# Kernel tuning notes

Measured on AMD Instinct MI355X. Metric: run time of the kernel, lower is better.

## Reference

```python
import jax, jax.numpy as jnp
import numpy as np
import math

ATTN_SCALE = 1.0 / math.sqrt(128.0)
NEG_INF = float(np.finfo(np.float32).min)


def get_slopes(n_heads: int) -> np.ndarray:
    # ALiBi head-specific slopes, geometric series; handles non-power-of-2 heads.
    n = 2 ** math.floor(math.log2(n_heads))
    m_0 = 2.0 ** (-8.0 / n)
    m = m_0 ** np.arange(1, 1 + n, dtype=np.float64)
    if n < n_heads:
        m_hat_0 = 2.0 ** (-4.0 / n)
        m_hat = m_hat_0 ** np.arange(1, 1 + 2 * (n_heads - n), 2, dtype=np.float64)
        m = np.concatenate([m, m_hat])
    return m.astype(np.float32).reshape(1, -1, 1, 1)  # [1, h, 1, 1]


def setup_inputs() -> dict:
    key = jax.random.key(0)
    kq, kk, kv = jax.random.split(key, 3)
    b, h, s, d = 4, 16, 2048, 128
    q = jax.random.normal(kq, (b, h, s, d), dtype=jnp.float32)
    k = jax.random.normal(kk, (b, h, s, d), dtype=jnp.float32)
    v = jax.random.normal(kv, (b, h, s, d), dtype=jnp.float32)
    return {"q": q, "k": k, "v": v}


def reference(q, k, v):
    b, h, s_q, d = q.shape
    s_kv = k.shape[2]
    # scores: [b, h, s_q, s_kv]
    s = jnp.einsum('bhqd,bhkd->bhqk', q, k) * ATTN_SCALE
    # ALiBi: (j - i) * slope_h, added after scaling
    rel = (jnp.arange(s_kv, dtype=q.dtype)[None, :]
           - jnp.arange(s_q, dtype=q.dtype)[:, None])  # [s_q, s_kv]
    slopes = jnp.asarray(get_slopes(h), dtype=q.dtype)  # [1, h, 1, 1]
    s = s + rel[None, None, :, :] * slopes
    # causal mask: positions j > i get -inf
    causal = jnp.arange(s_kv)[None, :] > jnp.arange(s_q)[:, None]  # [s_q, s_kv]
    s = jnp.where(causal[None, None, :, :], jnp.array(-jnp.inf, dtype=s.dtype), s)
    p = jax.nn.softmax(s, axis=-1)
    o = jnp.einsum('bhqk,bhkd->bhqd', p, v)
    return o
```

## Files before the change

### kernel.cpp

```cpp
#include <hip/hip_runtime.h>
#include <math.h>

#define S_LEN 2048
#define DHEAD 128
#define NHEAD 16
#define QBLK  256
#define KVBLK 64
#define ATT_SCALE 0.08838834764831845f
#define LOG2E 1.4426950408889634f
#define SHIFT2 11.5f

#define KP 136
#define VP 72

typedef __attribute__((ext_vector_type(4))) float f32x4;
typedef __attribute__((ext_vector_type(8))) short s16x8;
typedef __attribute__((ext_vector_type(2))) int   i32x2;

__device__ __forceinline__ int pk2(float lo, float hi) {
  int d;
  asm("v_cvt_pk_bf16_f32 %0, %1, %2" : "=v"(d) : "v"(lo), "v"(hi));
  return d;
}

#define BARRIER() do {                                   \
    asm volatile("s_waitcnt lgkmcnt(0)" ::: "memory");   \
    __builtin_amdgcn_s_barrier();                        \
  } while (0)


__global__ __launch_bounds__(512, 2)
void alibi_attn_fwd(const float* __restrict__ Qg, const float* __restrict__ Kg,
                    const float* __restrict__ Vg, float* __restrict__ Og)
{
  __shared__ __align__(16) short kt[2][KVBLK * KP];
  __shared__ __align__(16) short vt[3][DHEAD * VP];

  const int tid  = threadIdx.x;
  const int lane = tid & 63;
  const int w    = tid >> 6;
  const int l16  = lane & 15;
  const int lg   = lane >> 4;

  const int n    = blockIdx.x;
  const int bh   = n & 63;
  const int p    = n >> 6;
  const int head = bh & (NHEAD - 1);

  const size_t base = (size_t)bh * S_LEN * DHEAD;
  const float* Q = Qg + base;
  const float* K = Kg + base;
  const float* V = Vg + base;
  float*       O = Og + base;

  const float slope2 = exp2f(-0.5f * (float)(head + 1)) * LOG2E;
  float cn16[4], rsv[4];
  #pragma unroll
  for (int x = 0; x < 4; ++x) { cn16[x] = (float)(16 * x) * slope2; rsv[x] = (float)x * slope2; }

  s16x8 ones;
  #pragma unroll
  for (int jj = 0; jj < 8; ++jj) ones[jj] = (short)0x3f80;

  const f32x4 zero4 = {0.f, 0.f, 0.f, 0.f};

  const int qt0 = 7 - p, qt1 = p;
  const int qb0 = qt0 * QBLK, qb1 = qt1 * QBLK;
  const int n0  = 4 * (qt0 + 1);
  const int NT  = n0 + 4 * (qt1 + 1);

  const int kr  = tid >> 3;
  const int d0k = 16 * (tid & 7);
  const int grp = tid & 15, vnt = grp >> 2, vg = grp & 3;
  const int Rv  = 16 * vnt + 4 * vg;
  const int dv  = 4 * (tid >> 4);
  const int vslotb = 32 * (vnt >> 1) + 8 * vg + 4 * (vnt & 1);

  f32x4 ka[4], va[4];

#define LOAD_TILE(KV0) do {                                            \
    const float* kp_ = K + (size_t)((KV0) + kr) * DHEAD + d0k;         \
    ka[0] = *(const f32x4*)(kp_);      ka[1] = *(const f32x4*)(kp_ + 4);  \
    ka[2] = *(const f32x4*)(kp_ + 8);  ka[3] = *(const f32x4*)(kp_ + 12); \
    const float* vp_ = V + (size_t)((KV0) + Rv) * DHEAD + dv;          \
    va[0] = *(const f32x4*)(vp_);                                      \
    va[1] = *(const f32x4*)(vp_ + DHEAD);                              \
    va[2] = *(const f32x4*)(vp_ + 2*DHEAD);                            \
    va[3] = *(const f32x4*)(vp_ + 3*DHEAD);                            \
  } while (0)

#define STORE_TILE(BK, BV) do {                                        \
    short* ktp = &kt[BK][kr * KP + d0k];                               \
    union { int d[4]; s16x8 v; } u0, u1;                               \
    u0.d[0] = pk2(ka[0][0], ka[0][1]); u0.d[1] = pk2(ka[0][2], ka[0][3]); \
    u0.d[2] = pk2(ka[1][0], ka[1][1]); u0.d[3] = pk2(ka[1][2], ka[1][3]); \
    u1.d[0] = pk2(ka[2][0], ka[2][1]); u1.d[1] = pk2(ka[2][2], ka[2][3]); \
    u1.d[2] = pk2(ka[3][0], ka[3][1]); u1.d[3] = pk2(ka[3][2], ka[3][3]); \
    *(s16x8*)(ktp)     = u0.v;                                         \
    *(s16x8*)(ktp + 8) = u1.v;                                         \
    _Pragma("unroll")                                                  \
    for (int e = 0; e < 4; ++e) {                                      \
      i32x2 dvv;                                                       \
      dvv[0] = pk2(va[0][e], va[1][e]);                                \
      dvv[1] = pk2(va[2][e], va[3][e]);                                \
      *(i32x2*)&vt[BV][(dv + e) * VP + vslotb] = dvv;                  \
    }                                                                  \
  } while (0)

  s16x8 qf[2][4];
  f32x4 oacc[2][8], lacc[2];
  int   iq0 = 0;
  int   qb  = qb0;

  auto init_phase = [&](int qbn) {
    qb  = qbn;
    iq0 = qbn + 32 * w + l16;
    #pragma unroll
    for (int m = 0; m < 2; ++m) {
      const float* qp = Q + (size_t)(qbn + 32*w + 16*m + l16) * DHEAD + 8*lg;
      #pragma unroll
      for (int c = 0; c < 4; ++c) {
        f32x4 a = *(const f32x4*)(qp + 32*c);
        f32x4 b = *(const f32x4*)(qp + 32*c + 4);
        const float sc = ATT_SCALE * LOG2E;
        union { int d[4]; s16x8 v; } uu;
        uu.d[0] = pk2(a[0]*sc, a[1]*sc); uu.d[1] = pk2(a[2]*sc, a[3]*sc);
        uu.d[2] = pk2(b[0]*sc, b[1]*sc); uu.d[3] = pk2(b[2]*sc, b[3]*sc);
        qf[m][c] = uu.v;
      }
      #pragma unroll
      for (int dt = 0; dt < 8; ++dt) oacc[m][dt] = zero4;
      lacc[m] = zero4;
    }
  };

  auto epilogue = [&](int qbn) {
    #pragma unroll
    for (int m = 0; m < 2; ++m) {
      #pragma unroll
      for (int r = 0; r < 4; ++r) {
        const float inv = 1.0f / lacc[m][r];
        float* op = O + (size_t)(qbn + 32*w + 16*m + 4*lg + r) * DHEAD + l16;
        #pragma unroll
        for (int dt = 0; dt < 8; ++dt) op[dt * 16] = oacc[m][dt][r] * inv;
      }
    }
  };

  s16x8 pa[2][2];
  bool  pactive = false;

  auto pv_block = [&](const short* vtc) {
    __builtin_amdgcn_s_setprio(1);
    #pragma unroll
    for (int c2 = 0; c2 < 2; ++c2) {
      lacc[0] = __builtin_amdgcn_mfma_f32_16x16x32_bf16(pa[0][c2], ones, lacc[0], 0, 0, 0);
      lacc[1] = __builtin_amdgcn_mfma_f32_16x16x32_bf16(pa[1][c2], ones, lacc[1], 0, 0, 0);
      #pragma unroll
      for (int dt = 0; dt < 8; ++dt) {
        s16x8 bv = *(const s16x8*)&vtc[(dt*16 + l16) * VP + c2*32 + 8*lg];
        oacc[0][dt] = __builtin_amdgcn_mfma_f32_16x16x32_bf16(pa[0][c2], bv, oacc[0][dt], 0, 0, 0);
        oacc[1][dt] = __builtin_amdgcn_mfma_f32_16x16x32_bf16(pa[1][c2], bv, oacc[1][dt], 0, 0, 0);
      }
    }
    __builtin_amdgcn_s_setprio(0);
  };

  init_phase(qb0);
  LOAD_TILE(0);
  STORE_TILE(0, 0);
  LOAD_TILE(KVBLK);
  __syncthreads();

  for (int s = 0; s < NT; ++s) {
    if (s == n0) {
      if (pactive) pv_block(vt[(n0 - 1) % 3]);
      epilogue(qb0);
      init_phase(qb1);
      pactive = false;
    }
    const int kv0 = ((s < n0) ? s : s - n0) * KVBLK;

    if (s + 1 < NT) STORE_TILE((s + 1) & 1, (s + 1) % 3);

    const bool active = (kv0 <= qb + 32 * w + 31);

    f32x4 sacc[2][4];
    s16x8 pnew[2][2];
    if (active) {
      const short* ktc = kt[s & 1];
      #pragma unroll
      for (int nt = 0; nt < 4; ++nt) { sacc[0][nt] = zero4; sacc[1][nt] = zero4; }
      __builtin_amdgcn_s_setprio(1);
      #pragma unroll
      for (int c = 0; c < 4; ++c) {
        #pragma unroll
        for (int nt = 0; nt < 4; ++nt) {
          s16x8 kf = *(const s16x8*)&ktc[(nt*16 + l16) * KP + 32*c + 8*lg];
          sacc[0][nt] = __builtin_amdgcn_mfma_f32_16x16x32_bf16(kf, qf[0][c], sacc[0][nt], 0, 0, 0);
          sacc[1][nt] = __builtin_amdgcn_mfma_f32_16x16x32_bf16(kf, qf[1][c], sacc[1][nt], 0, 0, 0);
        }
      }
      __builtin_amdgcn_s_setprio(0);

      const bool needMask = (kv0 + KVBLK - 1 > qb + 32 * w);
      #pragma unroll
      for (int m = 0; m < 2; ++m) {
        const int dji = kv0 + 4*lg - (iq0 + 16*m);
        const float b0m = (float)dji * slope2 - SHIFT2;
        float pv[4][4];
        #pragma unroll
        for (int nt = 0; nt < 4; ++nt) {
          const float bmn = b0m + cn16[nt];
          #pragma unroll
          for (int r = 0; r < 4; ++r)
            pv[nt][r] = __builtin_amdgcn_exp2f(sacc[m][nt][r] + bmn + rsv[r]);
        }
        if (needMask) {
          #pragma unroll
          for (int nt = 0; nt < 4; ++nt)
            #pragma unroll
            for (int r = 0; r < 4; ++r)
              if (dji + 16*nt + r > 0) pv[nt][r] = 0.f;
        }
        #pragma unroll
        for (int c2 = 0; c2 < 2; ++c2) {
          union { int d[4]; s16x8 v; } uu;
          uu.d[0] = pk2(pv[2*c2][0],   pv[2*c2][1]);
          uu.d[1] = pk2(pv[2*c2][2],   pv[2*c2][3]);
          uu.d[2] = pk2(pv[2*c2+1][0], pv[2*c2+1][1]);
          uu.d[3] = pk2(pv[2*c2+1][2], pv[2*c2+1][3]);
          pnew[m][c2] = uu.v;
        }
      }
    }

    if (pactive) pv_block(vt[(s - 1) % 3]);

    if (active) {
      #pragma unroll
      for (int m = 0; m < 2; ++m)
        #pragma unroll
        for (int c2 = 0; c2 < 2; ++c2) pa[m][c2] = pnew[m][c2];
    }
    pactive = active;

    if (s + 2 < NT) {
      const int s2 = s + 2;
      LOAD_TILE(((s2 < n0) ? s2 : s2 - n0) * KVBLK);
    }

    BARRIER();
  }

  if (pactive) pv_block(vt[(NT - 1) % 3]);
  epilogue(qb1);
}

extern "C" void kernel_launch(void* const* d_in, const int* in_sizes, int n_in,
                              void* d_out, int out_size, void* d_ws, size_t ws_size,
                              hipStream_t stream) {
  (void)in_sizes; (void)n_in; (void)out_size; (void)d_ws; (void)ws_size;
  const float* q = (const float*)d_in[0];
  const float* k = (const float*)d_in[1];
  const float* v = (const float*)d_in[2];
  float* o = (float*)d_out;
  dim3 grid(256);
  dim3 block(512);
  alibi_attn_fwd<<<grid, block, 0, stream>>>(q, k, v, o);
}
```

Measured before the change: 109.0 us.

## Split warps into two phase-shifted groups for QK/softmax and PV overlap

Warps 0-3 now compute QK, softmax and PV for the same KV tile in one step. Warps 4-7 keep the software-pipelined order, running PV for the previous tile before QK of the current one. The two halves are out of phase, so MFMA and exp work from different warps can interleave on a CU and contend less for the same unit at the same moment. The custom barrier with an explicit lgkmcnt wait is replaced by __syncthreads. The triple-buffered V tile indexing is adjusted per group, which raises the risk of reading a stale buffer.

Result: no change. 108.7 us (-0.2%).

```diff
diff --git a/kernel.cpp b/kernel.cpp
--- a/kernel.cpp
+++ b/kernel.cpp
@@ -23,11 +23,6 @@
   return d;
 }
 
-#define BARRIER() do {                                   \
-    asm volatile("s_waitcnt lgkmcnt(0)" ::: "memory");   \
-    __builtin_amdgcn_s_barrier();                        \
-  } while (0)
-
 
 __global__ __launch_bounds__(512, 2)
 void alibi_attn_fwd(const float* __restrict__ Qg, const float* __restrict__ Kg,
@@ -41,6 +36,7 @@
   const int w    = tid >> 6;
   const int l16  = lane & 15;
   const int lg   = lane >> 4;
+  const bool isB = (w >= 4);
 
   const int n    = blockIdx.x;
   const int bh   = n & 63;
@@ -147,24 +143,72 @@
     }
   };
 
-  s16x8 pa[2][2];
-  bool  pactive = false;
-
-  auto pv_block = [&](const short* vtc) {
+  auto qk_sm = [&](const short* ktc, int kv0, s16x8 (&paO)[2][2]) {
+    f32x4 sacc[2][4];
+    #pragma unroll
+    for (int nt = 0; nt < 4; ++nt) { sacc[0][nt] = zero4; sacc[1][nt] = zero4; }
     __builtin_amdgcn_s_setprio(1);
     #pragma unroll
+    for (int c = 0; c < 4; ++c) {
+      #pragma unroll
+      for (int nt = 0; nt < 4; ++nt) {
+        s16x8 kf = *(const s16x8*)&ktc[(nt*16 + l16) * KP + 32*c + 8*lg];
+        sacc[0][nt] = __builtin_amdgcn_mfma_f32_16x16x32_bf16(kf, qf[0][c], sacc[0][nt], 0, 0, 0);
+        sacc[1][nt] = __builtin_amdgcn_mfma_f32_16x16x32_bf16(kf, qf[1][c], sacc[1][nt], 0, 0, 0);
+      }
+    }
+    __builtin_amdgcn_s_setprio(0);
+
+    const bool needMask = (kv0 + KVBLK - 1 > qb + 32 * w);
+    #pragma unroll
+    for (int m = 0; m < 2; ++m) {
+      const int dji = kv0 + 4*lg - (iq0 + 16*m);
+      const float b0m = (float)dji * slope2 - SHIFT2;
+      float pv[4][4];
+      #pragma unroll
+      for (int nt = 0; nt < 4; ++nt) {
+        const float bmn = b0m + cn16[nt];
+        #pragma unroll
+        for (int r = 0; r < 4; ++r)
+          pv[nt][r] = __builtin_amdgcn_exp2f(sacc[m][nt][r] + bmn + rsv[r]);
+      }
+      if (needMask) {
+        #pragma unroll
+        for (int nt = 0; nt < 4; ++nt)
+          #pragma unroll
+          for (int r = 0; r < 4; ++r)
+            if (dji + 16*nt + r > 0) pv[nt][r] = 0.f;
+      }
+      #pragma unroll
+      for (int c2 = 0; c2 < 2; ++c2) {
+        union { int d[4]; s16x8 v; } uu;
+        uu.d[0] = pk2(pv[2*c2][0],   pv[2*c2][1]);
+        uu.d[1] = pk2(pv[2*c2][2],   pv[2*c2][3]);
+        uu.d[2] = pk2(pv[2*c2+1][0], pv[2*c2+1][1]);
+        uu.d[3] = pk2(pv[2*c2+1][2], pv[2*c2+1][3]);
+        paO[m][c2] = uu.v;
+      }
+    }
+  };
+
+  auto pv_block = [&](const short* vtc, const s16x8 (&paI)[2][2]) {
+    __builtin_amdgcn_s_setprio(1);
+    #pragma unroll
     for (int c2 = 0; c2 < 2; ++c2) {
-      lacc[0] = __builtin_amdgcn_mfma_f32_16x16x32_bf16(pa[0][c2], ones, lacc[0], 0, 0, 0);
-      lacc[1] = __builtin_amdgcn_mfma_f32_16x16x32_bf16(pa[1][c2], ones, lacc[1], 0, 0, 0);
+      lacc[0] = __builtin_amdgcn_mfma_f32_16x16x32_bf16(paI[0][c2], ones, lacc[0], 0, 0, 0);
+      lacc[1] = __builtin_amdgcn_mfma_f32_16x16x32_bf16(paI[1][c2], ones, lacc[1], 0, 0, 0);
       #pragma unroll
       for (int dt = 0; dt < 8; ++dt) {
         s16x8 bv = *(const s16x8*)&vtc[(dt*16 + l16) * VP + c2*32 + 8*lg];
-        oacc[0][dt] = __builtin_amdgcn_mfma_f32_16x16x32_bf16(pa[0][c2], bv, oacc[0][dt], 0, 0, 0);
-        oacc[1][dt] = __builtin_amdgcn_mfma_f32_16x16x32_bf16(pa[1][c2], bv, oacc[1][dt], 0, 0, 0);
+        oacc[0][dt] = __builtin_amdgcn_mfma_f32_16x16x32_bf16(paI[0][c2], bv, oacc[0][dt], 0, 0, 0);
+        oacc[1][dt] = __builtin_amdgcn_mfma_f32_16x16x32_bf16(paI[1][c2], bv, oacc[1][dt], 0, 0, 0);
       }
     }
     __builtin_amdgcn_s_setprio(0);
   };
+
+  s16x8 pa[2][2];
+  bool  pend = false;
 
   init_phase(qb0);
   LOAD_TILE(0);
@@ -174,86 +218,33 @@
 
   for (int s = 0; s < NT; ++s) {
     if (s == n0) {
-      if (pactive) pv_block(vt[(n0 - 1) % 3]);
+      if (isB && pend) pv_block(vt[(n0 + 2) % 3], pa);
       epilogue(qb0);
       init_phase(qb1);
-      pactive = false;
-    }
-    const int kv0 = ((s < n0) ? s : s - n0) * KVBLK;
-
+      pend = false;
+    }
     if (s + 1 < NT) STORE_TILE((s + 1) & 1, (s + 1) % 3);
-
-    const bool active = (kv0 <= qb + 32 * w + 31);
-
-    f32x4 sacc[2][4];
-    s16x8 pnew[2][2];
-    if (active) {
-      const short* ktc = kt[s & 1];
-      #pragma unroll
-      for (int nt = 0; nt < 4; ++nt) { sacc[0][nt] = zero4; sacc[1][nt] = zero4; }
-      __builtin_amdgcn_s_setprio(1);
-      #pragma unroll
-      for (int c = 0; c < 4; ++c) {
-        #pragma unroll
-        for (int nt = 0; nt < 4; ++nt) {
-          s16x8 kf = *(const s16x8*)&ktc[(nt*16 + l16) * KP + 32*c + 8*lg];
-          sacc[0][nt] = __builtin_amdgcn_mfma_f32_16x16x32_bf16(kf, qf[0][c], sacc[0][nt], 0, 0, 0);
-          sacc[1][nt] = __builtin_amdgcn_mfma_f32_16x16x32_bf16(kf, qf[1][c], sacc[1][nt], 0, 0, 0);
-        }
-      }
-      __builtin_amdgcn_s_setprio(0);
-
-      const bool needMask = (kv0 + KVBLK - 1 > qb + 32 * w);
-      #pragma unroll
-      for (int m = 0; m < 2; ++m) {
-        const int dji = kv0 + 4*lg - (iq0 + 16*m);
-        const float b0m = (float)dji * slope2 - SHIFT2;
-        float pv[4][4];
-        #pragma unroll
-        for (int nt = 0; nt < 4; ++nt) {
-          const float bmn = b0m + cn16[nt];
-          #pragma unroll
-          for (int r = 0; r < 4; ++r)
-            pv[nt][r] = __builtin_amdgcn_exp2f(sacc[m][nt][r] + bmn + rsv[r]);
-        }
-        if (needMask) {
-          #pragma unroll
-          for (int nt = 0; nt < 4; ++nt)
-            #pragma unroll
-            for (int r = 0; r < 4; ++r)
-              if (dji + 16*nt + r > 0) pv[nt][r] = 0.f;
-        }
-        #pragma unroll
-        for (int c2 = 0; c2 < 2; ++c2) {
-          union { int d[4]; s16x8 v; } uu;
-          uu.d[0] = pk2(pv[2*c2][0],   pv[2*c2][1]);
-          uu.d[1] = pk2(pv[2*c2][2],   pv[2*c2][3]);
-          uu.d[2] = pk2(pv[2*c2+1][0], pv[2*c2+1][1]);
-          uu.d[3] = pk2(pv[2*c2+1][2], pv[2*c2+1][3]);
-          pnew[m][c2] = uu.v;
-        }
-      }
-    }
-
-    if (pactive) pv_block(vt[(s - 1) % 3]);
-
-    if (active) {
-      #pragma unroll
-      for (int m = 0; m < 2; ++m)
-        #pragma unroll
-        for (int c2 = 0; c2 < 2; ++c2) pa[m][c2] = pnew[m][c2];
-    }
-    pactive = active;
-
     if (s + 2 < NT) {
       const int s2 = s + 2;
       LOAD_TILE(((s2 < n0) ? s2 : s2 - n0) * KVBLK);
     }
-
-    BARRIER();
+    const int kv0 = ((s < n0) ? s : s - n0) * KVBLK;
+    const bool active = (kv0 <= qb + 32 * w + 31);
+
+    if (!isB) {
+      if (active) {
+        qk_sm(kt[s & 1], kv0, pa);
+        pv_block(vt[s % 3], pa);
+      }
+    } else {
+      if (pend) pv_block(vt[(s + 2) % 3], pa);
+      if (active) qk_sm(kt[s & 1], kv0, pa);
+      pend = active;
+    }
+
+    __syncthreads();
   }
-
-  if (pactive) pv_block(vt[(NT - 1) % 3]);
+  if (isB && pend) pv_block(vt[(NT + 2) % 3], pa);
   epilogue(qb1);
 }
 
```
